# Performance work log

Hardware: AMD Instinct MI355X
Metric: run time of the kernel (lower is better)

Reference implementation:

```python
import jax, jax.numpy as jnp
import numpy as np

IN_FEATURES = 1024
OUT_FEATURES = 1024
KNOT_COUNT = 5
ORDER = 3
BATCH = 4096


def setup_inputs() -> dict:
    key = jax.random.key(0)
    k1, k2 = jax.random.split(key)
    x = jax.random.normal(k1, (BATCH, IN_FEATURES), dtype=jnp.float32)
    knots = jnp.linspace(-1.0, 1.0, KNOT_COUNT, dtype=jnp.float32)
    coeffs = jax.random.normal(k2, (KNOT_COUNT + ORDER, OUT_FEATURES, IN_FEATURES), dtype=jnp.float32)
    return {"x": x, "knots": knots, "coeffs": coeffs}


def _bspline_bases(x, knots, order):
    # x: [B, I]; knots: [K] uniform grid. Extend to K + 2*order + 1 knots so
    # the number of degree-`order` basis functions is K + order.
    h = knots[1] - knots[0]
    left = knots[0] + h * jnp.arange(-order, 0, dtype=knots.dtype)
    right = knots[-1] + h * jnp.arange(1, order + 2, dtype=knots.dtype)
    t = jnp.concatenate([left, knots, right])  # [K + 2*order + 1]
    xe = x[..., None]  # [B, I, 1]
    # degree-0 indicator bases: [B, I, m-1]
    bases = ((xe >= t[:-1]) & (xe < t[1:])).astype(x.dtype)
    # Cox-de Boor recursion up to degree `order` (vectorized over batch/features)
    for k in range(1, order + 1):
        left_num = (xe - t[: -(k + 1)]) / (t[k:-1] - t[: -(k + 1)])
        right_num = (t[k + 1:] - xe) / (t[k + 1:] - t[1:-k])
        bases = left_num * bases[..., :-1] + right_num * bases[..., 1:]
    return bases  # [B, I, K + order]


def reference(x, knots, coeffs):
    # Faithful fused version of the per-(i,j) python loops:
    # spline_j(b) = sum_n B_n(x[b,i]) * coeffs[n, j, i]; output sums over i.
    bases = _bspline_bases(x, knots, ORDER)          # [B, I, N]
    return jnp.einsum('bin,noi->bo', bases, coeffs)  # [B, O]
```

## Files before the change

### kernel.cpp

```cpp
#include <hip/hip_runtime.h>
#include <hip/hip_bf16.h>
#include <cstdint>
#include <cstddef>

#define IN_F   1024
#define OUT_F  1024
#define NB     8
#define BATCH  4096
#define KTOT   (NB * IN_F)

typedef __attribute__((ext_vector_type(4))) float  f32x4;
typedef __attribute__((ext_vector_type(8))) float  f32x8;
typedef __attribute__((ext_vector_type(8))) __bf16 bf16x8;
typedef __attribute__((ext_vector_type(4))) unsigned short u16x4;

#define GLDS16(g, l)                                                     \
    __builtin_amdgcn_global_load_lds(                                    \
        (const __attribute__((address_space(1))) void*)(g),              \
        (__attribute__((address_space(3))) void*)(l), 16, 0, 0)

__device__ __forceinline__ void spline_w(float r, float w[4]) {
    const float r2 = r * r, r3 = r2 * r;
    const float omr = 1.0f - r;
    w[0] = omr * omr * omr * (1.0f / 6.0f);
    w[1] = (3.0f * r3 - 6.0f * r2 + 4.0f) * (1.0f / 6.0f);
    w[2] = (-3.0f * r3 + 3.0f * r2 + 3.0f * r + 1.0f) * (1.0f / 6.0f);
    w[3] = r3 * (1.0f / 6.0f);
}

__global__ void k_cvt(const float* __restrict__ src, __bf16* __restrict__ dst) {
    const size_t g   = blockIdx.x * blockDim.x + threadIdx.x;
    const size_t idx = g * 8;
    const int i = (int)(idx & 1023);
    const int o = (int)((idx >> 10) & 1023);
    const int c = (i >> 3) & 7;
    const int isw = (i & ~63) | ((c ^ (o & 7)) << 3);
    f32x8 v = *(const f32x8*)(src + idx);
    bf16x8 ov = __builtin_convertvector(v, bf16x8);
    *(bf16x8*)(dst + (idx - i) + isw) = ov;
}

__global__ void k_basis(const float* __restrict__ x, __bf16* __restrict__ A) {
    const int g    = blockIdx.x * blockDim.x + threadIdx.x;
    const int flat = g * 4;
    const int b = flat >> 10, i = flat & 1023;
    f32x4 xv = *(const f32x4*)(x + flat);

    float w[4][4];
    int   jj[4];
#pragma unroll
    for (int e = 0; e < 4; ++e) {
        const float u  = (xv[e] + 2.5f) * 2.0f;
        const float jf = floorf(u);
        jj[e] = (int)jf;
        spline_w(u - jf, w[e]);
    }

    const int c   = (i >> 3) & 7;
    const int isw = (i & ~63) | ((c ^ (b & 7)) << 3) | (i & 7);
    __bf16* base = A + (size_t)b * KTOT + isw;
#pragma unroll
    for (int n = 0; n < NB; ++n) {
        u16x4 pack;
#pragma unroll
        for (int e = 0; e < 4; ++e) {
            const int d = n - jj[e] + 3;
            float v = (d == 0) ? w[e][0]
                    : (d == 1) ? w[e][1]
                    : (d == 2) ? w[e][2]
                    : (d == 3) ? w[e][3] : 0.0f;
            __bf16 h = (__bf16)v;
            pack[e] = __builtin_bit_cast(unsigned short, h);
        }
        *(u16x4*)(base + n * IN_F) = pack;
    }
}

#define BM 256
#define BN 128
#define BK 64
#define NT (KTOT / BK)
#define SPLITK 2
#define NTS (NT / SPLITK)
#define BUFSZ 49152

__global__ __launch_bounds__(512) void k_gemm(const __bf16* __restrict__ A,
                                              const __bf16* __restrict__ W,
                                              float* __restrict__ C,
                                              float* __restrict__ P) {
    __shared__ __align__(16) char ls[3 * BUFSZ];

    const int fid = blockIdx.x;
    const int xcd = fid & 7;
    const int s   = fid >> 3;
    const int y   = xcd + 8 * (s & 1);
    const int xb  = (s >> 1) & 7;
    const int kz  = s >> 4;

    const int o0   = xb * BN;
    const int b0   = y * BM;
    const int tid  = threadIdx.x;
    const int lane = tid & 63;
    const int wv   = tid >> 6;
    const int wr   = wv >> 1;
    const int wc   = wv & 1;
    const int l15  = lane & 15;
    const int lhi  = lane >> 4;

    f32x4 acc[4][4] = {};

    const int srow  = tid >> 3;
    const int scol8 = (tid & 7) * 8;

    auto STAGE = [&](int buf, int kt) {
        const int k0 = kt * BK;
        const int n  = k0 >> 10;
        const int i0 = k0 & 1023;
        char* la = ls + buf * BUFSZ;
        char* lb = la + 32768;
#pragma unroll
        for (int it = 0; it < 4; ++it) {
            const __bf16* ga = A + (size_t)(b0 + srow + it * 64) * KTOT + k0 + scol8;
            GLDS16(ga, la + tid * 16 + it * 8192);
        }
#pragma unroll
        for (int it = 0; it < 2; ++it) {
            const __bf16* gw = W + ((size_t)n << 20)
                                 + (size_t)(o0 + srow + it * 64) * IN_F + i0 + scol8;
            GLDS16(gw, lb + tid * 16 + it * 8192);
        }
    };

    const int ktBeg = kz * NTS;
    STAGE(0, ktBeg);
    STAGE(1, ktBeg + 1);

    int cur = 0, nxt = 2;
    for (int t = 0; t < NTS; ++t) {
        if (t < NTS - 1) asm volatile("s_waitcnt vmcnt(6)" ::: "memory");
        else             asm volatile("s_waitcnt vmcnt(0)" ::: "memory");
        __builtin_amdgcn_s_barrier();
        __builtin_amdgcn_sched_barrier(0);

        if (t + 2 < NTS) STAGE(nxt, ktBeg + t + 2);

        const char* la = ls + cur * BUFSZ;
        const char* lb = la + 32768;
#pragma unroll
        for (int kk = 0; kk < BK; kk += 32) {
            bf16x8 af[4], bfr[4];
#pragma unroll
            for (int m = 0; m < 4; ++m) {
                const int r = wr * 64 + m * 16 + l15;
                const int c = ((kk >> 3) + lhi) ^ (r & 7);
                af[m] = *(const bf16x8*)(la + r * 128 + c * 16);
            }
#pragma unroll
            for (int nn = 0; nn < 4; ++nn) {
                const int r = wc * 64 + nn * 16 + l15;
                const int c = ((kk >> 3) + lhi) ^ (r & 7);
                bfr[nn] = *(const bf16x8*)(lb + r * 128 + c * 16);
            }
#pragma unroll
            for (int m = 0; m < 4; ++m)
#pragma unroll
                for (int nn = 0; nn < 4; ++nn)
                    acc[m][nn] = __builtin_amdgcn_mfma_f32_16x16x32_bf16(
                        af[m], bfr[nn], acc[m][nn], 0, 0, 0);
        }
        cur = (cur == 2) ? 0 : cur + 1;
        nxt = (nxt == 2) ? 0 : nxt + 1;
    }

    float* dst = (kz == 0) ? C : P;
    const int crow = lhi * 4;
#pragma unroll
    for (int m = 0; m < 4; ++m) {
#pragma unroll
        for (int nn = 0; nn < 4; ++nn) {
            float* cp = dst + (size_t)(b0 + wr * 64 + m * 16 + crow) * OUT_F
                            + o0 + wc * 64 + nn * 16 + l15;
#pragma unroll
            for (int j = 0; j < 4; ++j)
                cp[(size_t)j * OUT_F] = acc[m][nn][j];
        }
    }
}

__global__ void k_add(float* __restrict__ C, const float* __restrict__ P) {
    const size_t g = (size_t)(blockIdx.x * blockDim.x + threadIdx.x) * 4;
    f32x4 a = *(const f32x4*)(C + g);
    f32x4 b = *(const f32x4*)(P + g);
    a += b;
    *(f32x4*)(C + g) = a;
}

__global__ void k_naive(const float* __restrict__ x, const float* __restrict__ coeffs,
                        float* __restrict__ out) {
    const int b = blockIdx.y * 16 + (threadIdx.x >> 4);
    const int o = blockIdx.x * 16 + (threadIdx.x & 15);
    float sum = 0.0f;
    for (int i = 0; i < IN_F; ++i) {
        const float u  = (x[(size_t)b * IN_F + i] + 2.5f) * 2.0f;
        const float jf = floorf(u);
        const int   j  = (int)jf;
        float w[4];
        spline_w(u - jf, w);
#pragma unroll
        for (int m = 0; m < 4; ++m) {
            const int idx = j - 3 + m;
            if (idx >= 0 && idx < NB)
                sum += w[m] * coeffs[(size_t)idx * OUT_F * IN_F + (size_t)o * IN_F + i];
        }
    }
    out[(size_t)b * OUT_F + o] = sum;
}

extern "C" void kernel_launch(void* const* d_in, const int* in_sizes, int n_in,
                              void* d_out, int out_size, void* d_ws, size_t ws_size,
                              hipStream_t stream) {
    const float* x      = (const float*)d_in[0];
    const float* coeffs = (const float*)d_in[2];
    float* out = (float*)d_out;

    const size_t needA = (size_t)BATCH * KTOT * sizeof(__bf16);
    const size_t needW = (size_t)NB * OUT_F * IN_F * sizeof(__bf16);
    const size_t needP = (size_t)BATCH * OUT_F * sizeof(float);

    if (ws_size >= needA + needW + needP) {
        __bf16* A  = (__bf16*)d_ws;
        __bf16* Wb = (__bf16*)((char*)d_ws + needA);
        float*  P  = (float*)((char*)d_ws + needA + needW);

        hipLaunchKernelGGL(k_cvt, dim3(NB * OUT_F * IN_F / 8 / 256), dim3(256), 0,
                           stream, coeffs, Wb);
        hipLaunchKernelGGL(k_basis, dim3(BATCH * IN_F / 4 / 256), dim3(256), 0,
                           stream, x, A);
        hipLaunchKernelGGL(k_gemm, dim3(256), dim3(512), 0, stream, A, Wb, out, P);
        hipLaunchKernelGGL(k_add, dim3(BATCH * OUT_F / 4 / 256), dim3(256), 0,
                           stream, out, P);
    } else {
        hipLaunchKernelGGL(k_naive, dim3(OUT_F / 16, BATCH / 16), dim3(256), 0,
                           stream, x, coeffs, out);
    }
}
```

Baseline: 121.1 us.

## Fuse prep kernels, replace split-K partial buffer with atomic accumulation, add setprio

```diff
diff --git a/kernel.cpp b/kernel.cpp
--- a/kernel.cpp
+++ b/kernel.cpp
@@ -9,10 +9,9 @@
 #define BATCH  4096
 #define KTOT   (NB * IN_F)
 
-typedef __attribute__((ext_vector_type(4))) float  f32x4;
-typedef __attribute__((ext_vector_type(8))) float  f32x8;
-typedef __attribute__((ext_vector_type(8))) __bf16 bf16x8;
-typedef __attribute__((ext_vector_type(4))) unsigned short u16x4;
+typedef __attribute__((ext_vector_type(4)))  float  f32x4;
+typedef __attribute__((ext_vector_type(8)))  float  f32x8;
+typedef __attribute__((ext_vector_type(8)))  __bf16 bf16x8;
 
 #define GLDS16(g, l)                                                     \
     __builtin_amdgcn_global_load_lds(                                    \
@@ -28,51 +27,52 @@
     w[3] = r3 * (1.0f / 6.0f);
 }
 
-__global__ void k_cvt(const float* __restrict__ src, __bf16* __restrict__ dst) {
-    const size_t g   = blockIdx.x * blockDim.x + threadIdx.x;
-    const size_t idx = g * 8;
-    const int i = (int)(idx & 1023);
-    const int o = (int)((idx >> 10) & 1023);
-    const int c = (i >> 3) & 7;
-    const int isw = (i & ~63) | ((c ^ (o & 7)) << 3);
-    f32x8 v = *(const f32x8*)(src + idx);
-    bf16x8 ov = __builtin_convertvector(v, bf16x8);
-    *(bf16x8*)(dst + (idx - i) + isw) = ov;
-}
-
-__global__ void k_basis(const float* __restrict__ x, __bf16* __restrict__ A) {
-    const int g    = blockIdx.x * blockDim.x + threadIdx.x;
-    const int flat = g * 4;
-    const int b = flat >> 10, i = flat & 1023;
-    f32x4 xv = *(const f32x4*)(x + flat);
-
-    float w[4][4];
-    int   jj[4];
-#pragma unroll
-    for (int e = 0; e < 4; ++e) {
-        const float u  = (xv[e] + 2.5f) * 2.0f;
-        const float jf = floorf(u);
-        jj[e] = (int)jf;
-        spline_w(u - jf, w[e]);
-    }
-
-    const int c   = (i >> 3) & 7;
-    const int isw = (i & ~63) | ((c ^ (b & 7)) << 3) | (i & 7);
-    __bf16* base = A + (size_t)b * KTOT + isw;
-#pragma unroll
-    for (int n = 0; n < NB; ++n) {
-        u16x4 pack;
-#pragma unroll
-        for (int e = 0; e < 4; ++e) {
-            const int d = n - jj[e] + 3;
-            float v = (d == 0) ? w[e][0]
-                    : (d == 1) ? w[e][1]
-                    : (d == 2) ? w[e][2]
-                    : (d == 3) ? w[e][3] : 0.0f;
-            __bf16 h = (__bf16)v;
-            pack[e] = __builtin_bit_cast(unsigned short, h);
-        }
-        *(u16x4*)(base + n * IN_F) = pack;
+__global__ void k_prep(const float* __restrict__ coeffs, __bf16* __restrict__ Wb,
+                       const float* __restrict__ x, __bf16* __restrict__ A) {
+    const int bb = blockIdx.x;
+    if (bb < 4096) {
+        const size_t g   = (size_t)bb * blockDim.x + threadIdx.x;
+        const size_t idx = g * 8;
+        const int i = (int)(idx & 1023);
+        const int o = (int)((idx >> 10) & 1023);
+        const int c = (i >> 3) & 7;
+        const int isw = (i & ~63) | ((c ^ (o & 7)) << 3);
+        f32x8 v = *(const f32x8*)(coeffs + idx);
+        bf16x8 ov = __builtin_convertvector(v, bf16x8);
+        *(bf16x8*)(Wb + (idx - i) + isw) = ov;
+    } else {
+        const int g    = (bb - 4096) * blockDim.x + threadIdx.x;
+        const int flat = g * 8;
+        const int b = flat >> 10, i = flat & 1023;
+        f32x8 xv = *(const f32x8*)(x + flat);
+
+        float w[8][4];
+        int   jj[8];
+#pragma unroll
+        for (int e = 0; e < 8; ++e) {
+            const float u  = (xv[e] + 2.5f) * 2.0f;
+            const float jf = floorf(u);
+            jj[e] = (int)jf;
+            spline_w(u - jf, w[e]);
+        }
+
+        const int c   = (i >> 3) & 7;
+        const int isw = (i & ~63) | ((c ^ (b & 7)) << 3);
+        __bf16* base = A + (size_t)b * KTOT + isw;
+#pragma unroll
+        for (int n = 0; n < NB; ++n) {
+            bf16x8 pack;
+#pragma unroll
+            for (int e = 0; e < 8; ++e) {
+                const int d = n - jj[e] + 3;
+                float v = (d == 0) ? w[e][0]
+                        : (d == 1) ? w[e][1]
+                        : (d == 2) ? w[e][2]
+                        : (d == 3) ? w[e][3] : 0.0f;
+                pack[e] = (__bf16)v;
+            }
+            *(bf16x8*)(base + n * IN_F) = pack;
+        }
     }
 }
 
@@ -86,8 +86,7 @@
 
 __global__ __launch_bounds__(512) void k_gemm(const __bf16* __restrict__ A,
                                               const __bf16* __restrict__ W,
-                                              float* __restrict__ C,
-                                              float* __restrict__ P) {
+                                              float* __restrict__ C) {
     __shared__ __align__(16) char ls[3 * BUFSZ];
 
     const int fid = blockIdx.x;
@@ -161,38 +160,31 @@
                 const int c = ((kk >> 3) + lhi) ^ (r & 7);
                 bfr[nn] = *(const bf16x8*)(lb + r * 128 + c * 16);
             }
+            __builtin_amdgcn_s_setprio(1);
 #pragma unroll
             for (int m = 0; m < 4; ++m)
 #pragma unroll
                 for (int nn = 0; nn < 4; ++nn)
                     acc[m][nn] = __builtin_amdgcn_mfma_f32_16x16x32_bf16(
                         af[m], bfr[nn], acc[m][nn], 0, 0, 0);
+            __builtin_amdgcn_s_setprio(0);
         }
         cur = (cur == 2) ? 0 : cur + 1;
         nxt = (nxt == 2) ? 0 : nxt + 1;
     }
 
-    float* dst = (kz == 0) ? C : P;
     const int crow = lhi * 4;
 #pragma unroll
     for (int m = 0; m < 4; ++m) {
 #pragma unroll
         for (int nn = 0; nn < 4; ++nn) {
-            float* cp = dst + (size_t)(b0 + wr * 64 + m * 16 + crow) * OUT_F
-                            + o0 + wc * 64 + nn * 16 + l15;
+            float* cp = C + (size_t)(b0 + wr * 64 + m * 16 + crow) * OUT_F
+                          + o0 + wc * 64 + nn * 16 + l15;
 #pragma unroll
             for (int j = 0; j < 4; ++j)
-                cp[(size_t)j * OUT_F] = acc[m][nn][j];
-        }
-    }
-}
-
-__global__ void k_add(float* __restrict__ C, const float* __restrict__ P) {
-    const size_t g = (size_t)(blockIdx.x * blockDim.x + threadIdx.x) * 4;
-    f32x4 a = *(const f32x4*)(C + g);
-    f32x4 b = *(const f32x4*)(P + g);
-    a += b;
-    *(f32x4*)(C + g) = a;
+                unsafeAtomicAdd(cp + (size_t)j * OUT_F, acc[m][nn][j]);
+        }
+    }
 }
 
 __global__ void k_naive(const float* __restrict__ x, const float* __restrict__ coeffs,
@@ -225,20 +217,16 @@
 
     const size_t needA = (size_t)BATCH * KTOT * sizeof(__bf16);
     const size_t needW = (size_t)NB * OUT_F * IN_F * sizeof(__bf16);
-    const size_t needP = (size_t)BATCH * OUT_F * sizeof(float);
-
-    if (ws_size >= needA + needW + needP) {
+
+    if (ws_size >= needA + needW) {
         __bf16* A  = (__bf16*)d_ws;
         __bf16* Wb = (__bf16*)((char*)d_ws + needA);
-        float*  P  = (float*)((char*)d_ws + needA + needW);
-
-        hipLaunchKernelGGL(k_cvt, dim3(NB * OUT_F * IN_F / 8 / 256), dim3(256), 0,
-                           stream, coeffs, Wb);
-        hipLaunchKernelGGL(k_basis, dim3(BATCH * IN_F / 4 / 256), dim3(256), 0,
-                           stream, x, A);
-        hipLaunchKernelGGL(k_gemm, dim3(256), dim3(512), 0, stream, A, Wb, out, P);
-        hipLaunchKernelGGL(k_add, dim3(BATCH * OUT_F / 4 / 256), dim3(256), 0,
-                           stream, out, P);
+
+        hipMemsetAsync(out, 0, (size_t)BATCH * OUT_F * sizeof(float), stream);
+        hipLaunchKernelGGL(k_prep, dim3(6144), dim3(256), 0, stream,
+                           coeffs, Wb, x, A);
+        hipLaunchKernelGGL(k_gemm, dim3(256), dim3(512), 0, stream,
+                           A, Wb, out);
     } else {
         hipLaunchKernelGGL(k_naive, dim3(OUT_F / 16, BATCH / 16), dim3(256), 0,
                            stream, x, coeffs, out);
```

After: 137.3 us. 13.4% more time.
